# Kernel tuning notes

Measured on AMD Instinct MI355X. Metric: run time of the kernel, lower is better.

Reference implementation:

```python
import jax, jax.numpy as jnp
import numpy as np

MEMORY_COEF = 0.25
DHAT_COEF = 0.1

B, D, T, K = 64, 256, 512, 512
C, L = 8, 512


def setup_inputs() -> dict:
    key = jax.random.key(0)
    k1, k2, k3, k4, k5 = jax.random.split(key, 5)
    return {
        "Xhat": jax.random.normal(k1, (B, C, L), dtype=jnp.float32),
        "X": jax.random.normal(k2, (B, C, L), dtype=jnp.float32),
        "H": jax.random.normal(k3, (B, D, T), dtype=jnp.float32),
        "M": jax.random.normal(k4, (D, K), dtype=jnp.float32),
        "Dhat": jax.random.normal(k5, (B, T), dtype=jnp.float32),
    }


def _memory_loss(H, M):
    # H: [B, D, T]; M: [D, K] codebook with K codewords of dim D
    Ht = jnp.transpose(H, (0, 2, 1))  # [B, T, D]
    Mt = M.T                          # [K, D]
    # Squared distances via ||h||^2 - 2 h.m + ||m||^2 (argmin equals argmin of norms)
    d2 = (jnp.sum(Ht * Ht, axis=-1, keepdims=True)
          - 2.0 * jnp.einsum('btd,kd->btk', Ht, Mt)
          + jnp.sum(Mt * Mt, axis=-1))  # [B, T, K]
    idx = jnp.argmin(d2, axis=2)        # [B, T]
    Z = jnp.transpose(Mt[idx], (0, 2, 1))  # [B, D, T]
    sg = jax.lax.stop_gradient
    # ||.||^2 along dim D (norm then pow(2) == sum of squares)
    diffs = jnp.sum((sg(H) - Z) ** 2, axis=1) + jnp.sum((H - sg(Z)) ** 2, axis=1)  # [B, T]
    return jnp.sum(diffs) / float(np.prod(H.shape))


def reference(Xhat, X, H, M, Dhat):
    rec = jnp.mean((Xhat - X) ** 2)
    return rec + MEMORY_COEF * _memory_loss(H, M) - DHAT_COEF * jnp.mean(Dhat)
```

## Files before the change

kernel.cpp:

```cpp
#include <hip/hip_runtime.h>

#define NB   64
#define DD   256
#define TT   512
#define KK   512

typedef short bf8 __attribute__((ext_vector_type(8)));
typedef float f4  __attribute__((ext_vector_type(4)));

__device__ inline unsigned f2bf(float x) {
  unsigned u = __float_as_uint(x);
  u += 0x7FFFu + ((u >> 16) & 1u);
  return u >> 16;
}

#define MFMA(accv, va, vb) \
  asm("v_mfma_f32_16x16x32_bf16 %0, %1, %2, %0" : "+v"(accv) : "v"(va), "v"(vb))

#define ACCROW(acc, kt) \
    "+v"(acc[kt][0]), "+v"(acc[kt][1]), "+v"(acc[kt][2]), "+v"(acc[kt][3]), \
    "+v"(acc[kt][4]), "+v"(acc[kt][5]), "+v"(acc[kt][6]), "+v"(acc[kt][7])
#define ACCLIST8(acc) ACCROW(acc,0), ACCROW(acc,1), ACCROW(acc,2), ACCROW(acc,3)

#define GLOAD16(dst, src) \
  asm volatile("global_load_dwordx4 %0, %1, off" : "=v"(dst) : "v"(src))

__device__ inline void gload_lds16(const void* g, void* l) {
  __builtin_amdgcn_global_load_lds(
      (const __attribute__((address_space(1))) unsigned*)g,
      (__attribute__((address_space(3))) unsigned*)l, 16, 0, 0);
}

__global__ __launch_bounds__(256) void edm_prep(
    const float* __restrict__ M, const float4* __restrict__ Xh,
    const float4* __restrict__ X, const float4* __restrict__ Dh,
    unsigned short* __restrict__ MtF, float* __restrict__ mnorm,
    float* __restrict__ recp, float* __restrict__ dhp,
    unsigned* __restrict__ counter) {
  __shared__ __align__(16) float tile[DD][68];
  __shared__ float pn[4][64];
  __shared__ float ps[8];

  const int bid  = blockIdx.x;
  const int tid  = threadIdx.x;
  const int lane = tid & 63;
  const int q    = tid >> 6;

  if (bid == 0 && tid == 0) *counter = 0u;

  if (bid < 8) {
    #pragma unroll
    for (int it = 0; it < 16; ++it) {
      const int d  = q * 64 + it * 4 + (lane >> 4);
      const int kc = (lane & 15) << 2;
      *(float4*)&tile[d][kc] = *(const float4*)(M + (size_t)d * KK + bid * 64 + kc);
    }
    __syncthreads();
    const int k    = bid * 64 + lane;
    const int k16  = k >> 4;
    const int r16k = k & 15;
    float s = 0.f;
    #pragma unroll
    for (int dsl = 0; dsl < 2; ++dsl) {
      const int ds = q * 2 + dsl;
      #pragma unroll
      for (int g = 0; g < 4; ++g) {
        unsigned pk[4];
        #pragma unroll
        for (int e = 0; e < 4; ++e) {
          const float x0 = tile[ds * 32 + g * 8 + 2 * e + 0][lane];
          const float x1 = tile[ds * 32 + g * 8 + 2 * e + 1][lane];
          s += x0 * x0 + x1 * x1;
          pk[e] = f2bf(x0) | (f2bf(x1) << 16);
        }
        *(uint4*)(MtF + ((size_t)(k16 * 8 + ds) * 64 + r16k + 16 * g) * 8) =
            make_uint4(pk[0], pk[1], pk[2], pk[3]);
      }
    }
    pn[q][lane] = s;
    __syncthreads();
    if (q == 0) mnorm[k] = pn[0][lane] + pn[1][lane] + pn[2][lane] + pn[3][lane];
  } else {
    const int r = bid - 8;
    float s = 0.f, sd = 0.f;
    #pragma unroll
    for (int i = 0; i < 4; ++i) {
      const int idx = r * 1024 + i * 256 + tid;
      const float4 a = Xh[idx];
      const float4 c = X[idx];
      const float e0 = a.x - c.x, e1 = a.y - c.y, e2 = a.z - c.z, e3 = a.w - c.w;
      s += e0 * e0 + e1 * e1 + e2 * e2 + e3 * e3;
    }
    if (tid < 128) {
      const float4 dd = Dh[r * 128 + tid];
      sd = dd.x + dd.y + dd.z + dd.w;
    }
    #pragma unroll
    for (int off = 32; off > 0; off >>= 1) {
      s  += __shfl_down(s, off);
      sd += __shfl_down(sd, off);
    }
    if (lane == 0) { ps[q] = s; ps[4 + q] = sd; }
    __syncthreads();
    if (tid == 0) {
      recp[r] = ps[0] + ps[1] + ps[2] + ps[3];
      dhp[r]  = ps[4] + ps[5] + ps[6] + ps[7];
    }
  }
}

__global__ __launch_bounds__(512, 2) void edm_main(
    const float* __restrict__ H, const unsigned short* __restrict__ MtF,
    const float* __restrict__ mnorm, const float* __restrict__ recp,
    const float* __restrict__ dhp, float* __restrict__ d2part,
    unsigned* __restrict__ counter, float* __restrict__ out) {
  __shared__ __align__(16) float scratch[2][64][128];
  __shared__ __align__(16) unsigned short Hbf[128 * 256];
  __shared__ float hsum[128];
  __shared__ float wmin[8][128];
  __shared__ float red[12];
  __shared__ float bsum[2];
  __shared__ int   islast;

  const int tid  = threadIdx.x;
  const int wv   = tid >> 6;
  const int l    = tid & 63;
  const int tcol = tid & 127;
  const int q    = tid >> 7;
  const int r16  = l & 15;
  const int g    = l >> 4;

  const int b  = blockIdx.x >> 2;
  const int t0 = (blockIdx.x & 3) << 7;
  const float* Hb = H + (size_t)b * DD * TT + t0;

  if (tid < 128) hsum[tid] = 0.f;

  f4 acc[4][8];
  #pragma unroll
  for (int kt = 0; kt < 4; ++kt)
    #pragma unroll
    for (int tn = 0; tn < 8; ++tn)
      acc[kt][tn] = (f4){0.f, 0.f, 0.f, 0.f};
  asm volatile("s_nop 1" : ACCLIST8(acc));

  #define ISSUE_DMA(buf, ch)                                                  \
    {                                                                         \
      _Pragma("unroll")                                                       \
      for (int ii = 0; ii < 4; ++ii) {                                        \
        const int f  = ii * 512 + wv * 64;             \
        const int fl = f + l;                                                 \
        const int dl = fl >> 5;                                               \
        const int t4 = (fl & 31) << 2;                                        \
        gload_lds16(Hb + (size_t)((ch) * 64 + dl) * TT + t4,                  \
                    (char*)&scratch[buf][0][0] + (size_t)f * 16);             \
      }                                                                       \
    }

  ISSUE_DMA(0, 0);
  float hacc = 0.f;

  #pragma unroll
  for (int ch = 0; ch < 4; ++ch) {
    bf8 afr[2][4];
    #pragma unroll
    for (int s = 0; s < 2; ++s)
      #pragma unroll
      for (int kt = 0; kt < 4; ++kt)
        GLOAD16(afr[s][kt],
                (const void*)((const char*)MtF +
                              (((size_t)(wv * 4 + kt) * 8 + ch * 2 + s) * 64 + l) * 16));
    __builtin_amdgcn_sched_barrier(0);
    if (ch < 3) ISSUE_DMA((ch + 1) & 1, ch + 1);
    __builtin_amdgcn_sched_barrier(0);
    if (ch < 3) asm volatile("s_waitcnt vmcnt(12)" ::: "memory");
    else        asm volatile("s_waitcnt vmcnt(8)"  ::: "memory");
    __builtin_amdgcn_s_barrier();
    asm volatile("" ::: "memory");

    {
      unsigned wpk[8];
      #pragma unroll
      for (int jj = 0; jj < 8; ++jj) {
        const float x0 = scratch[ch & 1][q * 16 + 2 * jj + 0][tcol];
        const float x1 = scratch[ch & 1][q * 16 + 2 * jj + 1][tcol];
        hacc += x0 * x0 + x1 * x1;
        wpk[jj] = f2bf(x0) | (f2bf(x1) << 16);
      }
      char* rowp = (char*)Hbf + tcol * 512;
      const int dbase2 = (ch * 64 + q * 16) * 2;
      const int swz = (tcol & 7) << 4;
      *(uint4*)(rowp + ((dbase2 +  0) ^ swz)) = make_uint4(wpk[0], wpk[1], wpk[2], wpk[3]);
      *(uint4*)(rowp + ((dbase2 + 16) ^ swz)) = make_uint4(wpk[4], wpk[5], wpk[6], wpk[7]);
    }
    asm volatile("s_waitcnt lgkmcnt(0)" ::: "memory");
    __builtin_amdgcn_s_barrier();
    asm volatile("" ::: "memory");
    if (ch < 3) asm volatile("s_waitcnt vmcnt(4)" ::: "memory");
    else        asm volatile("s_waitcnt vmcnt(0)" ::: "memory");
    __builtin_amdgcn_sched_barrier(0);

    #pragma unroll
    for (int s = 0; s < 2; ++s) {
      const int ds = ch * 2 + s;
      #pragma unroll
      for (int tn = 0; tn < 8; ++tn) {
        const int t = tn * 16 + r16;
        const bf8 bfr = *(const bf8*)((const char*)Hbf + t * 512 +
                                      ((ds * 64 + g * 16) ^ ((t & 7) << 4)));
        MFMA(acc[0][tn], afr[s][0], bfr);
        MFMA(acc[1][tn], afr[s][1], bfr);
        MFMA(acc[2][tn], afr[s][2], bfr);
        MFMA(acc[3][tn], afr[s][3], bfr);
      }
    }
  }
  asm volatile("s_nop 7\n\ts_nop 7" : ACCLIST8(acc));

  atomicAdd(&hsum[tcol], hacc);

  float rmin[8] = {3.0e38f, 3.0e38f, 3.0e38f, 3.0e38f,
                   3.0e38f, 3.0e38f, 3.0e38f, 3.0e38f};
  #pragma unroll
  for (int kt = 0; kt < 4; ++kt) {
    const f4 mn = *(const f4*)(mnorm + wv * 64 + kt * 16 + g * 4);
    #pragma unroll
    for (int tn = 0; tn < 8; ++tn) {
      #pragma unroll
      for (int rr = 0; rr < 4; ++rr)
        rmin[tn] = fminf(rmin[tn], mn[rr] - 2.f * acc[kt][tn][rr]);
    }
  }
  #pragma unroll
  for (int tn = 0; tn < 8; ++tn) {
    rmin[tn] = fminf(rmin[tn], __shfl_xor(rmin[tn], 16));
    rmin[tn] = fminf(rmin[tn], __shfl_xor(rmin[tn], 32));
  }
  if (g == 0) {
    #pragma unroll
    for (int tn = 0; tn < 8; ++tn) wmin[wv][tn * 16 + r16] = rmin[tn];
  }
  __syncthreads();

  if (tid < 128) {
    float m = wmin[0][tid];
    #pragma unroll
    for (int w = 1; w < 8; ++w) m = fminf(m, wmin[w][tid]);
    float v = m + hsum[tid];
    #pragma unroll
    for (int off = 32; off > 0; off >>= 1) v += __shfl_down(v, off);
    if ((tid & 63) == 0) bsum[tid >> 6] = v;
  }
  __syncthreads();
  if (tid == 0) {
    __hip_atomic_store(&d2part[blockIdx.x], bsum[0] + bsum[1],
                       __ATOMIC_RELEASE, __HIP_MEMORY_SCOPE_AGENT);
    islast = (__hip_atomic_fetch_add(counter, 1u, __ATOMIC_ACQ_REL,
                                     __HIP_MEMORY_SCOPE_AGENT) == 255u) ? 1 : 0;
  }
  __syncthreads();

  if (islast) {
    float a = 0.f, r = 0.f, dh = 0.f;
    if (tid < 256) {
      a = __hip_atomic_load(&d2part[tid], __ATOMIC_RELAXED,
                            __HIP_MEMORY_SCOPE_AGENT);
      if (tid < 64) { r = recp[tid]; dh = dhp[tid]; }
    }
    #pragma unroll
    for (int off = 32; off > 0; off >>= 1) {
      a  += __shfl_down(a, off);
      r  += __shfl_down(r, off);
      dh += __shfl_down(dh, off);
    }
    if (tid < 256 && (tid & 63) == 0) {
      const int w = tid >> 6;
      red[w] = a; red[4 + w] = r; red[8 + w] = dh;
    }
    __syncthreads();
    if (tid == 0) {
      const float d2sum  = red[0] + red[1] + red[2] + red[3];
      const float recsum = red[4] + red[5] + red[6] + red[7];
      const float dhsum  = red[8] + red[9] + red[10] + red[11];
      out[0] = recsum * (1.f / 262144.f)
             + d2sum  * (1.f / 16777216.f)
             - 0.1f * dhsum * (1.f / 32768.f);
    }
  }
}

extern "C" void kernel_launch(void* const* d_in, const int* in_sizes, int n_in,
                              void* d_out, int out_size, void* d_ws, size_t ws_size,
                              hipStream_t stream) {
  const float* Xh = (const float*)d_in[0];
  const float* X  = (const float*)d_in[1];
  const float* H  = (const float*)d_in[2];
  const float* M  = (const float*)d_in[3];
  const float* Dh = (const float*)d_in[4];
  float* out = (float*)d_out;

  unsigned short* MtF = (unsigned short*)d_ws;
  float* mnorm = (float*)((char*)d_ws + (size_t)KK * DD * 2);
  float* recp  = mnorm + KK;
  float* dhp   = recp + 64;
  float* d2p   = dhp + 64;
  unsigned* counter = (unsigned*)(d2p + 256);

  edm_prep<<<72, 256, 0, stream>>>(M, (const float4*)Xh, (const float4*)X,
                                   (const float4*)Dh, MtF, mnorm, recp, dhp,
                                   counter);
  edm_main<<<NB * (TT / 128), 512, 0, stream>>>(H, MtF, mnorm, recp, dhp,
                                                d2p, counter, out);
}
```

Baseline: 29.50 us.

## Software-pipeline MFMA one chunk behind conversion and drop manual waitcnt scheduling

```diff
diff --git a/kernel.cpp b/kernel.cpp
--- a/kernel.cpp
+++ b/kernel.cpp
@@ -21,9 +21,6 @@
     "+v"(acc[kt][0]), "+v"(acc[kt][1]), "+v"(acc[kt][2]), "+v"(acc[kt][3]), \
     "+v"(acc[kt][4]), "+v"(acc[kt][5]), "+v"(acc[kt][6]), "+v"(acc[kt][7])
 #define ACCLIST8(acc) ACCROW(acc,0), ACCROW(acc,1), ACCROW(acc,2), ACCROW(acc,3)
-
-#define GLOAD16(dst, src) \
-  asm volatile("global_load_dwordx4 %0, %1, off" : "=v"(dst) : "v"(src))
 
 __device__ inline void gload_lds16(const void* g, void* l) {
   __builtin_amdgcn_global_load_lds(
@@ -116,7 +113,7 @@
     unsigned* __restrict__ counter, float* __restrict__ out) {
   __shared__ __align__(16) float scratch[2][64][128];
   __shared__ __align__(16) unsigned short Hbf[128 * 256];
-  __shared__ float hsum[128];
+  __shared__ float hsumP[4][128];
   __shared__ float wmin[8][128];
   __shared__ float red[12];
   __shared__ float bsum[2];
@@ -133,16 +130,6 @@
   const int b  = blockIdx.x >> 2;
   const int t0 = (blockIdx.x & 3) << 7;
   const float* Hb = H + (size_t)b * DD * TT + t0;
-
-  if (tid < 128) hsum[tid] = 0.f;
-
-  f4 acc[4][8];
-  #pragma unroll
-  for (int kt = 0; kt < 4; ++kt)
-    #pragma unroll
-    for (int tn = 0; tn < 8; ++tn)
-      acc[kt][tn] = (f4){0.f, 0.f, 0.f, 0.f};
-  asm volatile("s_nop 1" : ACCLIST8(acc));
 
   #define ISSUE_DMA(buf, ch)                                                  \
     {                                                                         \
@@ -157,33 +144,56 @@
       }                                                                       \
     }
 
+  f4 acc[4][8];
+  #pragma unroll
+  for (int kt = 0; kt < 4; ++kt)
+    #pragma unroll
+    for (int tn = 0; tn < 8; ++tn)
+      acc[kt][tn] = (f4){0.f, 0.f, 0.f, 0.f};
+  asm volatile("s_nop 1" : ACCLIST8(acc));
+
+  #define MFMA_CHUNK(cc)                                                      \
+    {                                                                         \
+      bf8 afr[2][4];                                                          \
+      _Pragma("unroll")                                                       \
+      for (int s = 0; s < 2; ++s)                                             \
+        _Pragma("unroll")                                                     \
+        for (int kt = 0; kt < 4; ++kt)                                        \
+          afr[s][kt] = *(const bf8*)(MtF +                                    \
+              (((size_t)(wv * 4 + kt) * 8 + (cc) * 2 + s) * 64 + l) * 8);     \
+      _Pragma("unroll")                                                       \
+      for (int s = 0; s < 2; ++s) {                                           \
+        const int ds = (cc) * 2 + s;                                          \
+        _Pragma("unroll")                                                     \
+        for (int tn = 0; tn < 8; ++tn) {                                      \
+          const int t = tn * 16 + r16;                                        \
+          const bf8 bfr = *(const bf8*)((const char*)Hbf + t * 512 +          \
+                              ((ds * 64 + g * 16) ^ ((t & 7) << 4)));         \
+          MFMA(acc[0][tn], afr[s][0], bfr);                                   \
+          MFMA(acc[1][tn], afr[s][1], bfr);                                   \
+          MFMA(acc[2][tn], afr[s][2], bfr);                                   \
+          MFMA(acc[3][tn], afr[s][3], bfr);                                   \
+        }                                                                     \
+      }                                                                       \
+    }
+
   ISSUE_DMA(0, 0);
+  __syncthreads();
+
   float hacc = 0.f;
-
   #pragma unroll
   for (int ch = 0; ch < 4; ++ch) {
-    bf8 afr[2][4];
-    #pragma unroll
-    for (int s = 0; s < 2; ++s)
-      #pragma unroll
-      for (int kt = 0; kt < 4; ++kt)
-        GLOAD16(afr[s][kt],
-                (const void*)((const char*)MtF +
-                              (((size_t)(wv * 4 + kt) * 8 + ch * 2 + s) * 64 + l) * 16));
-    __builtin_amdgcn_sched_barrier(0);
+    float xr[16];
+    #pragma unroll
+    for (int jj = 0; jj < 16; ++jj)
+      xr[jj] = scratch[ch & 1][q * 16 + jj][tcol];
     if (ch < 3) ISSUE_DMA((ch + 1) & 1, ch + 1);
-    __builtin_amdgcn_sched_barrier(0);
-    if (ch < 3) asm volatile("s_waitcnt vmcnt(12)" ::: "memory");
-    else        asm volatile("s_waitcnt vmcnt(8)"  ::: "memory");
-    __builtin_amdgcn_s_barrier();
-    asm volatile("" ::: "memory");
-
     {
       unsigned wpk[8];
       #pragma unroll
       for (int jj = 0; jj < 8; ++jj) {
-        const float x0 = scratch[ch & 1][q * 16 + 2 * jj + 0][tcol];
-        const float x1 = scratch[ch & 1][q * 16 + 2 * jj + 1][tcol];
+        const float x0 = xr[2 * jj + 0];
+        const float x1 = xr[2 * jj + 1];
         hacc += x0 * x0 + x1 * x1;
         wpk[jj] = f2bf(x0) | (f2bf(x1) << 16);
       }
@@ -193,31 +203,13 @@
       *(uint4*)(rowp + ((dbase2 +  0) ^ swz)) = make_uint4(wpk[0], wpk[1], wpk[2], wpk[3]);
       *(uint4*)(rowp + ((dbase2 + 16) ^ swz)) = make_uint4(wpk[4], wpk[5], wpk[6], wpk[7]);
     }
-    asm volatile("s_waitcnt lgkmcnt(0)" ::: "memory");
-    __builtin_amdgcn_s_barrier();
-    asm volatile("" ::: "memory");
-    if (ch < 3) asm volatile("s_waitcnt vmcnt(4)" ::: "memory");
-    else        asm volatile("s_waitcnt vmcnt(0)" ::: "memory");
-    __builtin_amdgcn_sched_barrier(0);
-
-    #pragma unroll
-    for (int s = 0; s < 2; ++s) {
-      const int ds = ch * 2 + s;
-      #pragma unroll
-      for (int tn = 0; tn < 8; ++tn) {
-        const int t = tn * 16 + r16;
-        const bf8 bfr = *(const bf8*)((const char*)Hbf + t * 512 +
-                                      ((ds * 64 + g * 16) ^ ((t & 7) << 4)));
-        MFMA(acc[0][tn], afr[s][0], bfr);
-        MFMA(acc[1][tn], afr[s][1], bfr);
-        MFMA(acc[2][tn], afr[s][2], bfr);
-        MFMA(acc[3][tn], afr[s][3], bfr);
-      }
-    }
-  }
+    if (ch > 0) MFMA_CHUNK(ch - 1);
+    __syncthreads();
+  }
+  MFMA_CHUNK(3);
   asm volatile("s_nop 7\n\ts_nop 7" : ACCLIST8(acc));
 
-  atomicAdd(&hsum[tcol], hacc);
+  hsumP[q][tcol] = hacc;
 
   float rmin[8] = {3.0e38f, 3.0e38f, 3.0e38f, 3.0e38f,
                    3.0e38f, 3.0e38f, 3.0e38f, 3.0e38f};
@@ -246,7 +238,7 @@
     float m = wmin[0][tid];
     #pragma unroll
     for (int w = 1; w < 8; ++w) m = fminf(m, wmin[w][tid]);
-    float v = m + hsum[tid];
+    float v = m + hsumP[0][tid] + hsumP[1][tid] + hsumP[2][tid] + hsumP[3][tid];
     #pragma unroll
     for (int off = 32; off > 0; off >>= 1) v += __shfl_down(v, off);
     if ((tid & 63) == 0) bsum[tid >> 6] = v;
```

Result: no change. 29.15 us (-1.2%).

## Replace pipelined async H staging with direct register loads before GEMM

Applied to the files above, without the earlier changes.

```diff
diff --git a/kernel.cpp b/kernel.cpp
--- a/kernel.cpp
+++ b/kernel.cpp
@@ -21,15 +21,6 @@
     "+v"(acc[kt][0]), "+v"(acc[kt][1]), "+v"(acc[kt][2]), "+v"(acc[kt][3]), \
     "+v"(acc[kt][4]), "+v"(acc[kt][5]), "+v"(acc[kt][6]), "+v"(acc[kt][7])
 #define ACCLIST8(acc) ACCROW(acc,0), ACCROW(acc,1), ACCROW(acc,2), ACCROW(acc,3)
-
-#define GLOAD16(dst, src) \
-  asm volatile("global_load_dwordx4 %0, %1, off" : "=v"(dst) : "v"(src))
-
-__device__ inline void gload_lds16(const void* g, void* l) {
-  __builtin_amdgcn_global_load_lds(
-      (const __attribute__((address_space(1))) unsigned*)g,
-      (__attribute__((address_space(3))) unsigned*)l, 16, 0, 0);
-}
 
 __global__ __launch_bounds__(256) void edm_prep(
     const float* __restrict__ M, const float4* __restrict__ Xh,
@@ -114,9 +105,8 @@
     const float* __restrict__ mnorm, const float* __restrict__ recp,
     const float* __restrict__ dhp, float* __restrict__ d2part,
     unsigned* __restrict__ counter, float* __restrict__ out) {
-  __shared__ __align__(16) float scratch[2][64][128];
   __shared__ __align__(16) unsigned short Hbf[128 * 256];
-  __shared__ float hsum[128];
+  __shared__ float hsumP[4][128];
   __shared__ float wmin[8][128];
   __shared__ float red[12];
   __shared__ float bsum[2];
@@ -132,9 +122,28 @@
 
   const int b  = blockIdx.x >> 2;
   const int t0 = (blockIdx.x & 3) << 7;
-  const float* Hb = H + (size_t)b * DD * TT + t0;
-
-  if (tid < 128) hsum[tid] = 0.f;
+  const float* Hcol = H + (size_t)b * DD * TT + t0 + tcol;
+
+  float hacc = 0.f;
+  char* rowp = (char*)Hbf + tcol * 512;
+  const int swz = (tcol & 7) << 4;
+  #pragma unroll
+  for (int r = 0; r < 4; ++r) {
+    float x[16];
+    #pragma unroll
+    for (int j = 0; j < 16; ++j)
+      x[j] = Hcol[(size_t)(q * 64 + r * 16 + j) * TT];
+    unsigned pk[8];
+    #pragma unroll
+    for (int e = 0; e < 8; ++e) {
+      hacc += x[2 * e] * x[2 * e] + x[2 * e + 1] * x[2 * e + 1];
+      pk[e] = f2bf(x[2 * e]) | (f2bf(x[2 * e + 1]) << 16);
+    }
+    const int dbyte = q * 128 + r * 32;
+    *(uint4*)(rowp + ((dbyte +  0) ^ swz)) = make_uint4(pk[0], pk[1], pk[2], pk[3]);
+    *(uint4*)(rowp + ((dbyte + 16) ^ swz)) = make_uint4(pk[4], pk[5], pk[6], pk[7]);
+  }
+  hsumP[q][tcol] = hacc;
 
   f4 acc[4][8];
   #pragma unroll
@@ -144,80 +153,26 @@
       acc[kt][tn] = (f4){0.f, 0.f, 0.f, 0.f};
   asm volatile("s_nop 1" : ACCLIST8(acc));
 
-  #define ISSUE_DMA(buf, ch)                                                  \
-    {                                                                         \
-      _Pragma("unroll")                                                       \
-      for (int ii = 0; ii < 4; ++ii) {                                        \
-        const int f  = ii * 512 + wv * 64;             \
-        const int fl = f + l;                                                 \
-        const int dl = fl >> 5;                                               \
-        const int t4 = (fl & 31) << 2;                                        \
-        gload_lds16(Hb + (size_t)((ch) * 64 + dl) * TT + t4,                  \
-                    (char*)&scratch[buf][0][0] + (size_t)f * 16);             \
-      }                                                                       \
-    }
-
-  ISSUE_DMA(0, 0);
-  float hacc = 0.f;
-
-  #pragma unroll
-  for (int ch = 0; ch < 4; ++ch) {
-    bf8 afr[2][4];
-    #pragma unroll
-    for (int s = 0; s < 2; ++s)
-      #pragma unroll
-      for (int kt = 0; kt < 4; ++kt)
-        GLOAD16(afr[s][kt],
-                (const void*)((const char*)MtF +
-                              (((size_t)(wv * 4 + kt) * 8 + ch * 2 + s) * 64 + l) * 16));
-    __builtin_amdgcn_sched_barrier(0);
-    if (ch < 3) ISSUE_DMA((ch + 1) & 1, ch + 1);
-    __builtin_amdgcn_sched_barrier(0);
-    if (ch < 3) asm volatile("s_waitcnt vmcnt(12)" ::: "memory");
-    else        asm volatile("s_waitcnt vmcnt(8)"  ::: "memory");
-    __builtin_amdgcn_s_barrier();
-    asm volatile("" ::: "memory");
-
-    {
-      unsigned wpk[8];
-      #pragma unroll
-      for (int jj = 0; jj < 8; ++jj) {
-        const float x0 = scratch[ch & 1][q * 16 + 2 * jj + 0][tcol];
-        const float x1 = scratch[ch & 1][q * 16 + 2 * jj + 1][tcol];
-        hacc += x0 * x0 + x1 * x1;
-        wpk[jj] = f2bf(x0) | (f2bf(x1) << 16);
-      }
-      char* rowp = (char*)Hbf + tcol * 512;
-      const int dbase2 = (ch * 64 + q * 16) * 2;
-      const int swz = (tcol & 7) << 4;
-      *(uint4*)(rowp + ((dbase2 +  0) ^ swz)) = make_uint4(wpk[0], wpk[1], wpk[2], wpk[3]);
-      *(uint4*)(rowp + ((dbase2 + 16) ^ swz)) = make_uint4(wpk[4], wpk[5], wpk[6], wpk[7]);
-    }
-    asm volatile("s_waitcnt lgkmcnt(0)" ::: "memory");
-    __builtin_amdgcn_s_barrier();
-    asm volatile("" ::: "memory");
-    if (ch < 3) asm volatile("s_waitcnt vmcnt(4)" ::: "memory");
-    else        asm volatile("s_waitcnt vmcnt(0)" ::: "memory");
-    __builtin_amdgcn_sched_barrier(0);
-
-    #pragma unroll
-    for (int s = 0; s < 2; ++s) {
-      const int ds = ch * 2 + s;
-      #pragma unroll
-      for (int tn = 0; tn < 8; ++tn) {
-        const int t = tn * 16 + r16;
-        const bf8 bfr = *(const bf8*)((const char*)Hbf + t * 512 +
-                                      ((ds * 64 + g * 16) ^ ((t & 7) << 4)));
-        MFMA(acc[0][tn], afr[s][0], bfr);
-        MFMA(acc[1][tn], afr[s][1], bfr);
-        MFMA(acc[2][tn], afr[s][2], bfr);
-        MFMA(acc[3][tn], afr[s][3], bfr);
-      }
+  __syncthreads();
+
+  #pragma unroll
+  for (int ds = 0; ds < 8; ++ds) {
+    bf8 afr[4];
+    #pragma unroll
+    for (int kt = 0; kt < 4; ++kt)
+      afr[kt] = *(const bf8*)(MtF + (((size_t)(wv * 4 + kt) * 8 + ds) * 64 + l) * 8);
+    #pragma unroll
+    for (int tn = 0; tn < 8; ++tn) {
+      const int t = tn * 16 + r16;
+      const bf8 bfr = *(const bf8*)((const char*)Hbf + t * 512 +
+                                    ((ds * 64 + g * 16) ^ ((t & 7) << 4)));
+      MFMA(acc[0][tn], afr[0], bfr);
+      MFMA(acc[1][tn], afr[1], bfr);
+      MFMA(acc[2][tn], afr[2], bfr);
+      MFMA(acc[3][tn], afr[3], bfr);
     }
   }
   asm volatile("s_nop 7\n\ts_nop 7" : ACCLIST8(acc));
-
-  atomicAdd(&hsum[tcol], hacc);
 
   float rmin[8] = {3.0e38f, 3.0e38f, 3.0e38f, 3.0e38f,
                    3.0e38f, 3.0e38f, 3.0e38f, 3.0e38f};
@@ -246,7 +201,7 @@
     float m = wmin[0][tid];
     #pragma unroll
     for (int w = 1; w < 8; ++w) m = fminf(m, wmin[w][tid]);
-    float v = m + hsum[tid];
+    float v = m + hsumP[0][tid] + hsumP[1][tid] + hsumP[2][tid] + hsumP[3][tid];
     #pragma unroll
     for (int off = 32; off > 0; off >>= 1) v += __shfl_down(v, off);
     if ((tid & 63) == 0) bsum[tid >> 6] = v;
```

After: 28.70 us. 1.03x faster.
